# Kernel optimization log

Hardware: AMD Instinct MI355X
Metric: run time of the kernel (lower is better)

## Reference

```python
import jax, jax.numpy as jnp
import numpy as np

NUM_FEATURES = 128
NUM_FILTERS = 128

def setup_inputs() -> dict:
    key = jax.random.key(0)
    k1, k2, k3, k4, k5 = jax.random.split(key, 5)
    B, N, F = 4, 2048, NUM_FEATURES
    x = jax.random.normal(k1, (B, N, F), dtype=jnp.float32)
    A = jax.random.normal(k2, (B, N, N), dtype=jnp.float32)
    # Conv1D(num_filters, kernel_size=1, use_bias=False) == per-node linear F -> filters
    W = jax.random.normal(k3, (F, NUM_FILTERS), dtype=jnp.float32) * (1.0 / np.sqrt(F))
    # self.a: Conv1D(1, kernel_size=1) with bias == linear filters -> 1 (shared for x_i and x_j)
    a_w = jax.random.normal(k4, (NUM_FILTERS, 1), dtype=jnp.float32) * (1.0 / np.sqrt(NUM_FILTERS))
    a_b = jax.random.normal(k5, (1,), dtype=jnp.float32) * 0.01
    bias = jnp.zeros((NUM_FILTERS,), dtype=jnp.float32)
    return {"x": x, "A": A, "W": W, "a_w": a_w, "a_b": a_b, "bias": bias}

def reference(x, A, W, a_w, a_b, bias):
    # project features: [B,N,F] @ [F,Ff] -> [B,N,Ff]
    h = jnp.einsum('bnf,fg->bng', x, W)
    # shared attention projection (x_i and x_j use the same layer): [B,N,1]
    s = jnp.einsum('bng,go->bno', h, a_w) + a_b
    # additive scores s_i + s_j^T -> [B,N,N]
    e = s + jnp.swapaxes(s, 1, 2)
    e = jnp.where(e >= 0, e, 0.2 * e)  # LeakyReLU(0.2)
    attn = jax.nn.softmax(e + A, axis=-1)
    out = jnp.einsum('bij,bjg->big', attn, h) + bias
    return out
```

## Files before the change

kernel.cpp:

```cpp
#include <hip/hip_runtime.h>
#include <hip/hip_bf16.h>
#include <stdint.h>

#define BB 4
#define NN 2048
#define FF 128

typedef __attribute__((ext_vector_type(8))) short bf16x8;
typedef __attribute__((ext_vector_type(4))) float f32x4;

__device__ inline unsigned pk_bf16(float a, float b) {
    union { float f; unsigned u; } x, y;
    x.f = a; y.f = b;
    unsigned xu = x.u + (0x7fffu + ((x.u >> 16) & 1u));
    unsigned yu = y.u + (0x7fffu + ((y.u >> 16) & 1u));
    return (xu >> 16) | (yu & 0xffff0000u);
}

__device__ inline void glds16(const void* g, void* l) {
    __builtin_amdgcn_global_load_lds((const __attribute__((address_space(1))) void*)g,
                                     (__attribute__((address_space(3))) void*)l, 16, 0, 0);
}

#define XT_P 136
#define WT_P 136

__global__ __launch_bounds__(256) void k1_proj(
    const float* __restrict__ x, const float* __restrict__ W,
    const float* __restrict__ a_w, const float* __restrict__ a_b,
    uint16_t* __restrict__ Ht, float* __restrict__ s_out)
{
    __shared__ uint16_t xt[16 * XT_P];
    __shared__ uint16_t Wt[128 * WT_P];
    __shared__ float sredw[4 * 16];

    const int t = threadIdx.x;
    const int w = t >> 6, l = t & 63;
    const int m16 = l & 15, q = l >> 4;
    const int b = blockIdx.x >> 7;
    const int n0 = (blockIdx.x & 127) << 4;

    const int c4 = (t & 31) * 4, kh = (t >> 5) * 16;
    float4 wr0[8], wr1[8];
    #pragma unroll
    for (int kk = 0; kk < 8; ++kk) {
        const int k = kh + 2 * kk;
        wr0[kk] = *(const float4*)(W + (size_t)k * 128 + c4);
        wr1[kk] = *(const float4*)(W + (size_t)(k + 1) * 128 + c4);
    }
    {
        const int row = t >> 4, c0 = (t & 15) * 8;
        const float* xr = x + ((size_t)(b * NN + n0 + row)) * FF + c0;
        const float4 v0 = *(const float4*)xr;
        const float4 v1 = *(const float4*)(xr + 4);
        unsigned* dst = (unsigned*)(xt + row * XT_P + c0);
        dst[0] = pk_bf16(v0.x, v0.y); dst[1] = pk_bf16(v0.z, v0.w);
        dst[2] = pk_bf16(v1.x, v1.y); dst[3] = pk_bf16(v1.z, v1.w);
    }
    #pragma unroll
    for (int kk = 0; kk < 8; ++kk) {
        const int k = kh + 2 * kk;
        *(unsigned*)(Wt + (c4 + 0) * WT_P + k) = pk_bf16(wr0[kk].x, wr1[kk].x);
        *(unsigned*)(Wt + (c4 + 1) * WT_P + k) = pk_bf16(wr0[kk].y, wr1[kk].y);
        *(unsigned*)(Wt + (c4 + 2) * WT_P + k) = pk_bf16(wr0[kk].z, wr1[kk].z);
        *(unsigned*)(Wt + (c4 + 3) * WT_P + k) = pk_bf16(wr0[kk].w, wr1[kk].w);
    }
    const int g0 = (2 * w) * 16 + m16, g1 = (2 * w + 1) * 16 + m16;
    const float aw0 = a_w[g0], aw1 = a_w[g1];
    __syncthreads();

    f32x4 acc0 = {}, acc1 = {};
    bf16x8 af[4];
    #pragma unroll
    for (int dk = 0; dk < 4; ++dk)
        af[dk] = *(const bf16x8*)(xt + m16 * XT_P + dk * 32 + q * 8);
    #pragma unroll
    for (int dk = 0; dk < 4; ++dk) {
        bf16x8 b0 = *(const bf16x8*)(Wt + g0 * WT_P + dk * 32 + q * 8);
        bf16x8 b1 = *(const bf16x8*)(Wt + g1 * WT_P + dk * 32 + q * 8);
        acc0 = __builtin_amdgcn_mfma_f32_16x16x32_bf16(af[dk], b0, acc0, 0, 0, 0);
        acc1 = __builtin_amdgcn_mfma_f32_16x16x32_bf16(af[dk], b1, acc1, 0, 0, 0);
    }

    float sp[4];
    #pragma unroll
    for (int r = 0; r < 4; ++r) sp[r] = acc0[r] * aw0 + acc1[r] * aw1;
    #pragma unroll
    for (int off = 1; off < 16; off <<= 1)
        #pragma unroll
        for (int r = 0; r < 4; ++r) sp[r] += __shfl_xor(sp[r], off, 64);
    if (m16 == 0) {
        #pragma unroll
        for (int r = 0; r < 4; ++r) sredw[w * 16 + q * 4 + r] = sp[r];
    }
    {
        uint2 o0 = { pk_bf16(acc0[0], acc0[1]), pk_bf16(acc0[2], acc0[3]) };
        uint2 o1 = { pk_bf16(acc1[0], acc1[1]), pk_bf16(acc1[2], acc1[3]) };
        *(uint2*)(Ht + ((size_t)(b * 128 + g0)) * NN + n0 + q * 4) = o0;
        *(uint2*)(Ht + ((size_t)(b * 128 + g1)) * NN + n0 + q * 4) = o1;
    }
    __syncthreads();
    if (t < 16)
        s_out[b * NN + n0 + t] = sredw[t] + sredw[16 + t] + sredw[32 + t] + sredw[48 + t] + a_b[0];
}

#define JR 64
#define NR (NN / JR)
#define HT_GRP 1040
#define HT_TILE (16 * HT_GRP)
#define AT_P 68

__global__ __launch_bounds__(256, 2) void k2_attn(
    const float* __restrict__ A, const uint16_t* __restrict__ Ht,
    const float* __restrict__ s, const float* __restrict__ bias,
    float* __restrict__ out)
{
    __shared__ uint8_t htb[2][HT_TILE];
    __shared__ float atb[2][16 * AT_P];
    __shared__ float Op[16 * 132];
    __shared__ float rsums[16];
    __shared__ float rsp[2 * 64];

    const int t = threadIdx.x;
    const int w = t >> 6, l = t & 63;
    const int m16 = l & 15, q = l >> 4;
    const int wo = w & 1, gh = w >> 1;
    const int b = blockIdx.x >> 7;
    const int i0 = (blockIdx.x & 127) << 4;

    for (int i = t; i < 16 * 132; i += 256) Op[i] = 0.f;

    const float* sb = s + b * NN;
    const float* Ab = A + (size_t)b * NN * NN;
    const uint16_t* Hb = Ht + (size_t)b * 128 * NN;
    const float si = sb[i0 + m16];
    const float* Ast = Ab + (size_t)(i0 + (t >> 4)) * NN + (t & 15) * 4;
    const int sjo = q * 16 + wo * 8;

    #pragma unroll
    for (int u = 0; u < 4; ++u) {
        const int gg = w * 4 + u;
        glds16(Hb + (size_t)(gg * 8 + (l >> 3)) * NN + (l & 7) * 8, htb[0] + gg * HT_GRP);
    }
    {
        float4 a0 = *(const float4*)Ast;
        *(float4*)&atb[0][(t >> 4) * AT_P + (t & 15) * 4] = a0;
    }
    float4 sj0 = *(const float4*)(sb + sjo);
    float4 sj1 = *(const float4*)(sb + sjo + 4);
    __syncthreads();

    f32x4 acc[4] = {};
    float rs = 0.f;

    for (int r = 0; r < NR; ++r) {
        const int cur = r & 1, nxt = cur ^ 1;
        const int j1 = ((r + 1) & (NR - 1)) * JR;

        #pragma unroll
        for (int u = 0; u < 4; ++u) {
            const int gg = w * 4 + u;
            glds16(Hb + (size_t)(gg * 8 + (l >> 3)) * NN + j1 + (l & 7) * 8,
                   htb[nxt] + gg * HT_GRP);
        }
        float4 na = *(const float4*)(Ast + j1);
        float4 ns0 = *(const float4*)(sb + j1 + sjo);
        float4 ns1 = *(const float4*)(sb + j1 + sjo + 4);

        const float* ar = &atb[cur][m16 * AT_P + sjo];
        float4 af0 = *(const float4*)ar;
        float4 af1 = *(const float4*)(ar + 4);
        const float sjv[8] = {sj0.x, sj0.y, sj0.z, sj0.w, sj1.x, sj1.y, sj1.z, sj1.w};
        const float avv[8] = {af0.x, af0.y, af0.z, af0.w, af1.x, af1.y, af1.z, af1.w};
        float p[8];
        #pragma unroll
        for (int j = 0; j < 8; ++j) {
            float e = si + sjv[j];
            e = fmaxf(e, 0.2f * e);
            p[j] = __expf(e + avv[j]);
            rs += p[j];
        }
        union { unsigned u[4]; bf16x8 v; } fa;
        #pragma unroll
        for (int j = 0; j < 4; ++j) fa.u[j] = pk_bf16(p[2 * j], p[2 * j + 1]);

        #pragma unroll
        for (int t4 = 0; t4 < 4; ++t4) {
            const int g = gh * 64 + t4 * 16 + m16;
            const uint16_t* hp = (const uint16_t*)(htb[cur] + (g >> 3) * HT_GRP + (g & 7) * 128) + sjo;
            bf16x8 hb = *(const bf16x8*)hp;
            acc[t4] = __builtin_amdgcn_mfma_f32_16x16x32_bf16(fa.v, hb, acc[t4], 0, 0, 0);
        }

        *(float4*)&atb[nxt][(t >> 4) * AT_P + (t & 15) * 4] = na;
        sj0 = ns0; sj1 = ns1;
        __syncthreads();
    }

    if (w < 2) rsp[w * 64 + l] = rs;

    #pragma unroll
    for (int t4 = 0; t4 < 4; ++t4)
        #pragma unroll
        for (int r2 = 0; r2 < 4; ++r2)
            atomicAdd(&Op[(q * 4 + r2) * 132 + gh * 64 + t4 * 16 + m16], acc[t4][r2]);
    __syncthreads();

    if (t < 16) {
        float sum = 0.f;
        #pragma unroll
        for (int w2 = 0; w2 < 2; ++w2)
            #pragma unroll
            for (int q2 = 0; q2 < 4; ++q2)
                sum += rsp[w2 * 64 + q2 * 16 + t];
        rsums[t] = sum;
    }
    __syncthreads();

    {
        const int g = t & 127, rh = t >> 7;
        #pragma unroll
        for (int p2 = 0; p2 < 8; ++p2) {
            const int row = rh * 8 + p2;
            out[((size_t)b * NN + i0 + row) * FF + g] = Op[row * 132 + g] / rsums[row] + bias[g];
        }
    }
}

extern "C" void kernel_launch(void* const* d_in, const int* in_sizes, int n_in,
                              void* d_out, int out_size, void* d_ws, size_t ws_size,
                              hipStream_t stream) {
    const float* x    = (const float*)d_in[0];
    const float* A    = (const float*)d_in[1];
    const float* W    = (const float*)d_in[2];
    const float* a_w  = (const float*)d_in[3];
    const float* a_b  = (const float*)d_in[4];
    const float* bias = (const float*)d_in[5];
    float* out = (float*)d_out;

    uint16_t* Ht = (uint16_t*)d_ws;
    float* s = (float*)((char*)d_ws + (size_t)BB * 128 * NN * 2);

    k1_proj<<<BB * (NN / 16), 256, 0, stream>>>(x, W, a_w, a_b, Ht, s);
    k2_attn<<<BB * (NN / 16), 256, 0, stream>>>(A, Ht, s, bias, out);
}
```

Baseline: 145.5 us.

## Split attention over j-slices with LDS-resident H tiles and separate reduction kernel

The attention kernel is restructured as a split-K scheme. Each block covers 256 rows of i and one of 8 slices of j, and keeps the 256×128 bf16 H slice resident in XOR-swizzled LDS, so H no longer has to be streamed for every row group. Each block writes bf16 partial outputs and fp32 partial row sums to workspace, and a new third kernel sums the 8 slices, normalizes and adds bias. This trades the repeated H reads for extra global traffic on the partials, an additional launch, bf16 rounding of partial sums, and roughly 100KB of LDS per block, which limits occupancy to one block per CU.

New measurement: 141.8 us. 2.6% less time.

```diff
diff --git a/kernel.cpp b/kernel.cpp
--- a/kernel.cpp
+++ b/kernel.cpp
@@ -16,7 +16,10 @@
     unsigned yu = y.u + (0x7fffu + ((y.u >> 16) & 1u));
     return (xu >> 16) | (yu & 0xffff0000u);
 }
-
+__device__ inline uint16_t b16(float v) {
+    union { float f; unsigned u; } c; c.f = v;
+    return (uint16_t)((c.u + (0x7fffu + ((c.u >> 16) & 1u))) >> 16);
+}
 __device__ inline void glds16(const void* g, void* l) {
     __builtin_amdgcn_global_load_lds((const __attribute__((address_space(1))) void*)g,
                                      (__attribute__((address_space(3))) void*)l, 16, 0, 0);
@@ -104,127 +107,151 @@
         s_out[b * NN + n0 + t] = sredw[t] + sredw[16 + t] + sredw[32 + t] + sredw[48 + t] + a_b[0];
 }
 
-#define JR 64
-#define NR (NN / JR)
-#define HT_GRP 1040
-#define HT_TILE (16 * HT_GRP)
-#define AT_P 68
-
-__global__ __launch_bounds__(256, 2) void k2_attn(
+#define JS 8
+#define JRR 256
+#define NRND 16
+
+__global__ __launch_bounds__(256) void k2_attn(
     const float* __restrict__ A, const uint16_t* __restrict__ Ht,
-    const float* __restrict__ s, const float* __restrict__ bias,
-    float* __restrict__ out)
+    const float* __restrict__ s, uint16_t* __restrict__ po,
+    float* __restrict__ prs)
 {
-    __shared__ uint8_t htb[2][HT_TILE];
-    __shared__ float atb[2][16 * AT_P];
-    __shared__ float Op[16 * 132];
-    __shared__ float rsums[16];
-    __shared__ float rsp[2 * 64];
+    __shared__ uint16_t hts[128 * 256];
+    __shared__ float abuf[2][16 * 256];
+    __shared__ uint16_t pbuf[16 * 256];
+    __shared__ float rsLds[256];
 
     const int t = threadIdx.x;
     const int w = t >> 6, l = t & 63;
     const int m16 = l & 15, q = l >> 4;
-    const int wo = w & 1, gh = w >> 1;
-    const int b = blockIdx.x >> 7;
-    const int i0 = (blockIdx.x & 127) << 4;
-
-    for (int i = t; i < 16 * 132; i += 256) Op[i] = 0.f;
+
+    const int bx = blockIdx.x;
+    const int is = bx & 7;
+    const int js = (bx >> 3) & 7;
+    const int b  = bx >> 6;
+    const int j0 = js * JRR;
+    const int i0 = is * 256;
 
     const float* sb = s + b * NN;
     const float* Ab = A + (size_t)b * NN * NN;
-    const uint16_t* Hb = Ht + (size_t)b * 128 * NN;
-    const float si = sb[i0 + m16];
-    const float* Ast = Ab + (size_t)(i0 + (t >> 4)) * NN + (t & 15) * 4;
-    const int sjo = q * 16 + wo * 8;
-
+    const uint16_t* Hb = Ht + (size_t)b * FF * NN;
+
+    const int jA = 2 * w * 32 + q * 8;
+    float4 sj0 = *(const float4*)(sb + j0 + jA);
+    float4 sj1 = *(const float4*)(sb + j0 + jA + 4);
+    float4 sj2 = *(const float4*)(sb + j0 + jA + 32);
+    float4 sj3 = *(const float4*)(sb + j0 + jA + 36);
+
+    #pragma unroll
+    for (int u = 0; u < 16; ++u) {
+        const int row = 32 * w + 2 * u + (l >> 5);
+        const int c = l & 31;
+        glds16(Hb + (size_t)row * NN + j0 + 8 * (c ^ (row & 7)),
+               hts + (32 * w + 2 * u) * 256);
+    }
     #pragma unroll
     for (int u = 0; u < 4; ++u) {
-        const int gg = w * 4 + u;
-        glds16(Hb + (size_t)(gg * 8 + (l >> 3)) * NN + (l & 7) * 8, htb[0] + gg * HT_GRP);
-    }
-    {
-        float4 a0 = *(const float4*)Ast;
-        *(float4*)&atb[0][(t >> 4) * AT_P + (t & 15) * 4] = a0;
-    }
-    float4 sj0 = *(const float4*)(sb + sjo);
-    float4 sj1 = *(const float4*)(sb + sjo + 4);
+        const int row = 4 * w + u;
+        glds16(Ab + (size_t)(i0 + row) * NN + j0 + 4 * (l ^ (row & 7)),
+               &abuf[0][row * 256]);
+    }
     __syncthreads();
 
-    f32x4 acc[4] = {};
-    float rs = 0.f;
-
-    for (int r = 0; r < NR; ++r) {
+    for (int r = 0; r < NRND; ++r) {
         const int cur = r & 1, nxt = cur ^ 1;
-        const int j1 = ((r + 1) & (NR - 1)) * JR;
+        const int rn = (r + 1) & (NRND - 1);
 
         #pragma unroll
         for (int u = 0; u < 4; ++u) {
-            const int gg = w * 4 + u;
-            glds16(Hb + (size_t)(gg * 8 + (l >> 3)) * NN + j1 + (l & 7) * 8,
-                   htb[nxt] + gg * HT_GRP);
-        }
-        float4 na = *(const float4*)(Ast + j1);
-        float4 ns0 = *(const float4*)(sb + j1 + sjo);
-        float4 ns1 = *(const float4*)(sb + j1 + sjo + 4);
-
-        const float* ar = &atb[cur][m16 * AT_P + sjo];
-        float4 af0 = *(const float4*)ar;
-        float4 af1 = *(const float4*)(ar + 4);
-        const float sjv[8] = {sj0.x, sj0.y, sj0.z, sj0.w, sj1.x, sj1.y, sj1.z, sj1.w};
-        const float avv[8] = {af0.x, af0.y, af0.z, af0.w, af1.x, af1.y, af1.z, af1.w};
-        float p[8];
-        #pragma unroll
-        for (int j = 0; j < 8; ++j) {
-            float e = si + sjv[j];
+            const int row = 4 * w + u;
+            glds16(Ab + (size_t)(i0 + rn * 16 + row) * NN + j0 + 4 * (l ^ (row & 7)),
+                   &abuf[nxt][row * 256]);
+        }
+        const float si = sb[i0 + r * 16 + m16];
+
+        const int ga0 = (2 * w) * 8 + 2 * q;
+        const int ga1 = (2 * w + 1) * 8 + 2 * q;
+        const float* ac = &abuf[cur][m16 * 256];
+        const int x7 = m16 & 7;
+        float4 a0 = *(const float4*)(ac + 4 * (ga0 ^ x7));
+        float4 a1 = *(const float4*)(ac + 4 * ((ga0 + 1) ^ x7));
+        float4 a2 = *(const float4*)(ac + 4 * (ga1 ^ x7));
+        float4 a3 = *(const float4*)(ac + 4 * ((ga1 + 1) ^ x7));
+
+        const float sv[16] = {sj0.x,sj0.y,sj0.z,sj0.w, sj1.x,sj1.y,sj1.z,sj1.w,
+                              sj2.x,sj2.y,sj2.z,sj2.w, sj3.x,sj3.y,sj3.z,sj3.w};
+        const float av[16] = {a0.x,a0.y,a0.z,a0.w, a1.x,a1.y,a1.z,a1.w,
+                              a2.x,a2.y,a2.z,a2.w, a3.x,a3.y,a3.z,a3.w};
+        float pv[16]; float rs = 0.f;
+        #pragma unroll
+        for (int j = 0; j < 16; ++j) {
+            float e = si + sv[j];
             e = fmaxf(e, 0.2f * e);
-            p[j] = __expf(e + avv[j]);
-            rs += p[j];
-        }
-        union { unsigned u[4]; bf16x8 v; } fa;
-        #pragma unroll
-        for (int j = 0; j < 4; ++j) fa.u[j] = pk_bf16(p[2 * j], p[2 * j + 1]);
-
-        #pragma unroll
-        for (int t4 = 0; t4 < 4; ++t4) {
-            const int g = gh * 64 + t4 * 16 + m16;
-            const uint16_t* hp = (const uint16_t*)(htb[cur] + (g >> 3) * HT_GRP + (g & 7) * 128) + sjo;
-            bf16x8 hb = *(const bf16x8*)hp;
-            acc[t4] = __builtin_amdgcn_mfma_f32_16x16x32_bf16(fa.v, hb, acc[t4], 0, 0, 0);
-        }
-
-        *(float4*)&atb[nxt][(t >> 4) * AT_P + (t & 15) * 4] = na;
-        sj0 = ns0; sj1 = ns1;
+            pv[j] = __expf(e + av[j]);
+            rs += pv[j];
+        }
+        union { unsigned u[4]; bf16x8 v; } pk0, pk1;
+        #pragma unroll
+        for (int j = 0; j < 4; ++j) {
+            pk0.u[j] = pk_bf16(pv[2 * j], pv[2 * j + 1]);
+            pk1.u[j] = pk_bf16(pv[8 + 2 * j], pv[9 + 2 * j]);
+        }
+        *(bf16x8*)(pbuf + m16 * 256 + 8 * ((8 * w + q) ^ x7)) = pk0.v;
+        *(bf16x8*)(pbuf + m16 * 256 + 8 * ((8 * w + 4 + q) ^ x7)) = pk1.v;
+        rsLds[t] = rs;
         __syncthreads();
-    }
-
-    if (w < 2) rsp[w * 64 + l] = rs;
-
-    #pragma unroll
-    for (int t4 = 0; t4 < 4; ++t4)
-        #pragma unroll
-        for (int r2 = 0; r2 < 4; ++r2)
-            atomicAdd(&Op[(q * 4 + r2) * 132 + gh * 64 + t4 * 16 + m16], acc[t4][r2]);
-    __syncthreads();
-
-    if (t < 16) {
-        float sum = 0.f;
-        #pragma unroll
-        for (int w2 = 0; w2 < 2; ++w2)
+
+        f32x4 acc0 = {}, acc1 = {};
+        const int gA = w * 32 + m16, gB = w * 32 + 16 + m16;
+        #pragma unroll
+        for (int kk = 0; kk < 8; ++kk) {
+            const int jc = kk * 4 + q;
+            bf16x8 af = *(const bf16x8*)(pbuf + m16 * 256 + 8 * (jc ^ x7));
+            bf16x8 h0 = *(const bf16x8*)(hts + gA * 256 + 8 * (jc ^ x7));
+            bf16x8 h1 = *(const bf16x8*)(hts + gB * 256 + 8 * (jc ^ x7));
+            acc0 = __builtin_amdgcn_mfma_f32_16x16x32_bf16(af, h0, acc0, 0, 0, 0);
+            acc1 = __builtin_amdgcn_mfma_f32_16x16x32_bf16(af, h1, acc1, 0, 0, 0);
+        }
+
+        if (t < 16) {
+            float sum = 0.f;
             #pragma unroll
-            for (int q2 = 0; q2 < 4; ++q2)
-                sum += rsp[w2 * 64 + q2 * 16 + t];
-        rsums[t] = sum;
-    }
-    __syncthreads();
-
-    {
-        const int g = t & 127, rh = t >> 7;
-        #pragma unroll
-        for (int p2 = 0; p2 < 8; ++p2) {
-            const int row = rh * 8 + p2;
-            out[((size_t)b * NN + i0 + row) * FF + g] = Op[row * 132 + g] / rsums[row] + bias[g];
-        }
-    }
+            for (int w2 = 0; w2 < 4; ++w2)
+                #pragma unroll
+                for (int q2 = 0; q2 < 4; ++q2)
+                    sum += rsLds[w2 * 64 + q2 * 16 + t];
+            prs[(size_t)(js * BB + b) * NN + i0 + r * 16 + t] = sum;
+        }
+
+        const size_t pob = ((size_t)(js * BB + b) * NN + i0 + r * 16) * FF;
+        #pragma unroll
+        for (int rr = 0; rr < 4; ++rr) {
+            const int irow = q * 4 + rr;
+            po[pob + (size_t)irow * FF + w * 32 + m16]      = b16(acc0[rr]);
+            po[pob + (size_t)irow * FF + w * 32 + 16 + m16] = b16(acc1[rr]);
+        }
+        __syncthreads();
+    }
+}
+
+__global__ __launch_bounds__(256) void k3_red(
+    const uint16_t* __restrict__ po, const float* __restrict__ prs,
+    const float* __restrict__ bias, float* __restrict__ out)
+{
+    const int idx = blockIdx.x * 256 + threadIdx.x;
+    const int g = idx & 127;
+    const int i = (idx >> 7) & (NN - 1);
+    const int b = idx >> 18;
+    float sum = 0.f, rsum = 0.f;
+    #pragma unroll
+    for (int js = 0; js < JS; ++js) {
+        const size_t base = (size_t)(js * BB + b) * NN + i;
+        union { unsigned u; float f; } cv;
+        cv.u = ((unsigned)po[base * FF + g]) << 16;
+        sum += cv.f;
+        rsum += prs[base];
+    }
+    out[idx] = sum / rsum + bias[g];
 }
 
 extern "C" void kernel_launch(void* const* d_in, const int* in_sizes, int n_in,
@@ -238,9 +265,13 @@
     const float* bias = (const float*)d_in[5];
     float* out = (float*)d_out;
 
-    uint16_t* Ht = (uint16_t*)d_ws;
-    float* s = (float*)((char*)d_ws + (size_t)BB * 128 * NN * 2);
+    char* ws = (char*)d_ws;
+    uint16_t* Ht = (uint16_t*)ws;
+    float* s = (float*)(ws + 2 * 1024 * 1024);
+    uint16_t* po = (uint16_t*)(ws + 2 * 1024 * 1024 + 65536);
+    float* prs = (float*)(ws + 2 * 1024 * 1024 + 65536 + (size_t)JS * BB * NN * FF * 2);
 
     k1_proj<<<BB * (NN / 16), 256, 0, stream>>>(x, W, a_w, a_b, Ht, s);
-    k2_attn<<<BB * (NN / 16), 256, 0, stream>>>(A, Ht, s, bias, out);
-}
+    k2_attn<<<BB * 8 * 8, 256, 0, stream>>>(A, Ht, s, po, prs);
+    k3_red<<<(BB * NN * FF) / 256, 256, 0, stream>>>(po, prs, bias, out);
+}
```
